# Kernel tuning notes

Hardware: AMD Instinct MI355X
Metric: run time of the kernel (lower is better)

The kernel has to match this reference:

```python
import jax, jax.numpy as jnp
import numpy as np

HIDDEN = 1024
N_HEADS = 16
HEAD = HIDDEN // N_HEADS  # 64
DFF = 4 * HIDDEN


def setup_inputs() -> dict:
    key = jax.random.key(0)
    ks = jax.random.split(key, 12)
    B, T = 4, 2048
    s = 0.02
    return {
        "x": jax.random.normal(ks[0], (B, T, HIDDEN), jnp.float32),
        # per-head QKV weights, stacked: [H, HIDDEN, HEAD] (no bias, as in Head)
        "Wq": jax.random.normal(ks[1], (N_HEADS, HIDDEN, HEAD), jnp.float32) * s,
        "Wk": jax.random.normal(ks[2], (N_HEADS, HIDDEN, HEAD), jnp.float32) * s,
        "Wv": jax.random.normal(ks[3], (N_HEADS, HIDDEN, HEAD), jnp.float32) * s,
        "Wo": jax.random.normal(ks[4], (HIDDEN, HIDDEN), jnp.float32) * s,
        "bo": jnp.zeros((HIDDEN,), jnp.float32),
        "W1": jax.random.normal(ks[5], (HIDDEN, DFF), jnp.float32) * s,
        "b1": jnp.zeros((DFF,), jnp.float32),
        "W2": jax.random.normal(ks[6], (DFF, HIDDEN), jnp.float32) * s,
        "b2": jnp.zeros((HIDDEN,), jnp.float32),
        "g1": jnp.ones((HIDDEN,), jnp.float32),
        "be1": jnp.zeros((HIDDEN,), jnp.float32),
        "g2": jnp.ones((HIDDEN,), jnp.float32),
        "be2": jnp.zeros((HIDDEN,), jnp.float32),
    }


def _layernorm(x, g, b, eps=1e-5):
    mu = jnp.mean(x, axis=-1, keepdims=True)
    var = jnp.mean(jnp.square(x - mu), axis=-1, keepdims=True)
    return (x - mu) * jax.lax.rsqrt(var + eps) * g + b


def _attention(h, Wq, Wk, Wv, Wo, bo):
    B, T, C = h.shape
    # [B,T,C] x [H,C,D] -> [B,H,T,D]
    Q = jnp.einsum('btc,hcd->bhtd', h, Wq)
    K = jnp.einsum('btc,hcd->bhtd', h, Wk)
    V = jnp.einsum('btc,hcd->bhtd', h, Wv)
    scores = jnp.einsum('bhtd,bhsd->bhts', Q, K) / np.sqrt(HEAD).astype(np.float32)
    causal = jnp.tril(jnp.ones((T, T), bool))
    scores = jnp.where(causal, scores, -jnp.inf)
    attn = jax.nn.softmax(scores, axis=-1)
    out = jnp.einsum('bhts,bhsd->bhtd', attn, V)
    # concat heads in order (head axis -> last dim blocks)
    out = out.transpose(0, 2, 1, 3).reshape(B, T, C)
    return out @ Wo + bo


def reference(x, Wq, Wk, Wv, Wo, bo, W1, b1, W2, b2, g1, be1, g2, be2):
    x = x + _attention(_layernorm(x, g1, be1), Wq, Wk, Wv, Wo, bo)
    h = _layernorm(x, g2, be2)
    ff = jax.nn.relu(h @ W1 + b1) @ W2 + b2
    return x + ff
```

## Files before the change

### kernel.cpp

```cpp
#include <hip/hip_runtime.h>
#include <hip/hip_bf16.h>
#include <stdint.h>


#define HID 1024
#define NH 16
#define HD 64
#define DFF 4096
#define BATCH 4
#define SEQ 2048
#define NTOK (BATCH*SEQ)

typedef unsigned short u16;
typedef __attribute__((ext_vector_type(4))) float f32x4;
typedef __attribute__((ext_vector_type(8))) __bf16 bf16x8;

__device__ __forceinline__ u16 f2bf(float f) {
    unsigned int u = __float_as_uint(f);
    u = (u + 0x7fffu + ((u >> 16) & 1u)) >> 16;
    return (u16)u;
}

__device__ __forceinline__ void gload_lds16(const void* g, void* lds) {
    __builtin_amdgcn_global_load_lds(
        (const __attribute__((address_space(1))) unsigned int*)(uintptr_t)g,
        (__attribute__((address_space(3))) unsigned int*)(uintptr_t)lds, 16, 0, 0);
}

__global__ __launch_bounds__(256) void ln_kernel(const float* __restrict__ x,
                                                 const float* __restrict__ g,
                                                 const float* __restrict__ be,
                                                 u16* __restrict__ out) {
    __shared__ float red[10];
    const int row = blockIdx.x, tid = threadIdx.x;
    const float4 v = ((const float4*)(x + (size_t)row * HID))[tid];
    float s  = v.x + v.y + v.z + v.w;
    float s2 = v.x*v.x + v.y*v.y + v.z*v.z + v.w*v.w;
    for (int off = 32; off > 0; off >>= 1) {
        s  += __shfl_down(s, off, 64);
        s2 += __shfl_down(s2, off, 64);
    }
    if ((tid & 63) == 0) { red[tid >> 6] = s; red[4 + (tid >> 6)] = s2; }
    __syncthreads();
    if (tid == 0) {
        red[8] = red[0] + red[1] + red[2] + red[3];
        red[9] = red[4] + red[5] + red[6] + red[7];
    }
    __syncthreads();
    const float mu  = red[8] * (1.f / HID);
    const float var = red[9] * (1.f / HID) - mu * mu;
    const float rstd = rsqrtf(var + 1e-5f);
    const float4 g4 = ((const float4*)g)[tid];
    const float4 b4 = ((const float4*)be)[tid];
    ushort4 o;
    o.x = f2bf((v.x - mu) * rstd * g4.x + b4.x);
    o.y = f2bf((v.y - mu) * rstd * g4.y + b4.y);
    o.z = f2bf((v.z - mu) * rstd * g4.z + b4.z);
    o.w = f2bf((v.w - mu) * rstd * g4.w + b4.w);
    ((ushort4*)(out + (size_t)row * HID))[tid] = o;
}

__global__ __launch_bounds__(256) void transpose_w(const float* __restrict__ in,
                                                   u16* __restrict__ out, int R, int C) {
    __shared__ float t[32][33];
    const int r0 = blockIdx.x * 32, c0 = blockIdx.y * 32;
    const float* inb = in + (size_t)blockIdx.z * R * C;
    u16* outb = out + (size_t)blockIdx.z * R * C;
    const int tid = threadIdx.x;
    const int tr = tid >> 3, tc = (tid & 7) * 4;
    const float4 v = *(const float4*)&inb[(size_t)(r0 + tr) * C + c0 + tc];
    t[tr][tc] = v.x; t[tr][tc + 1] = v.y; t[tr][tc + 2] = v.z; t[tr][tc + 3] = v.w;
    __syncthreads();
    ushort4 o;
    o.x = f2bf(t[tc + 0][tr]);
    o.y = f2bf(t[tc + 1][tr]);
    o.z = f2bf(t[tc + 2][tr]);
    o.w = f2bf(t[tc + 3][tr]);
    *(ushort4*)&outb[(size_t)(c0 + tr) * R + r0 + tc] = o;
}

__global__ __launch_bounds__(256) void transpose_v(const u16* __restrict__ in,
                                                   u16* __restrict__ out) {
    __shared__ u16 t[64][65];
    const int s0 = blockIdx.x * 64;
    const size_t bh = blockIdx.y;
    const u16* inb = in + bh * SEQ * HD;
    u16* outb = out + bh * HD * SEQ;
    const int tid = threadIdx.x;
    const int r = tid >> 2, c = (tid & 3) * 16;
    bf16x8 a = *(const bf16x8*)&inb[(size_t)(s0 + r) * HD + c];
    bf16x8 b = *(const bf16x8*)&inb[(size_t)(s0 + r) * HD + c + 8];
    #pragma unroll
    for (int i = 0; i < 8; i++) {
        t[r][c + i]     = ((const u16*)&a)[i];
        t[r][c + 8 + i] = ((const u16*)&b)[i];
    }
    __syncthreads();
    u16 o0[8], o1[8];
    #pragma unroll
    for (int i = 0; i < 8; i++) { o0[i] = t[c + i][r]; o1[i] = t[c + 8 + i][r]; }
    *(bf16x8*)&outb[(size_t)r * SEQ + s0 + c]     = *(const bf16x8*)o0;
    *(bf16x8*)&outb[(size_t)r * SEQ + s0 + c + 8] = *(const bf16x8*)o1;
}

template <int MODE>
__global__ __launch_bounds__(256) void gemm_kernel(const u16* __restrict__ A,
                                                   const u16* __restrict__ B,
                                                   float* __restrict__ outf,
                                                   u16* __restrict__ outh,
                                                   const float* __restrict__ bias,
                                                   const float* __restrict__ resid,
                                                   int K, int N, float scale) {
    __shared__ u16 Al[128][32];
    __shared__ u16 Bl[128][32];
    const int tid = threadIdx.x;
    const int w = tid >> 6, l = tid & 63;
    const int wr = w >> 1, wc = w & 1;
    const int m0 = blockIdx.x * 128, n0 = blockIdx.y * 128;

    f32x4 acc[4][4] = {};

    const u16* Ag = A + (size_t)(m0 + w * 32) * K;
    const u16* Bg = B + (size_t)(n0 + w * 32) * K;
    const int lr = l >> 2;
    const int lc = (l & 3) * 8;

    for (int k0 = 0; k0 < K; k0 += 32) {
        __syncthreads();
        #pragma unroll
        for (int it = 0; it < 2; it++) {
            gload_lds16(Ag + (size_t)(it * 16 + lr) * K + k0 + lc, &Al[w * 32 + it * 16][0]);
            gload_lds16(Bg + (size_t)(it * 16 + lr) * K + k0 + lc, &Bl[w * 32 + it * 16][0]);
        }
        __syncthreads();
        bf16x8 af[4], bf[4];
        #pragma unroll
        for (int i = 0; i < 4; i++)
            af[i] = *(const bf16x8*)&Al[wr * 64 + i * 16 + (l & 15)][(l >> 4) * 8];
        #pragma unroll
        for (int i = 0; i < 4; i++)
            bf[i] = *(const bf16x8*)&Bl[wc * 64 + i * 16 + (l & 15)][(l >> 4) * 8];
        #pragma unroll
        for (int mi = 0; mi < 4; mi++)
            #pragma unroll
            for (int nj = 0; nj < 4; nj++)
                acc[mi][nj] = __builtin_amdgcn_mfma_f32_16x16x32_bf16(af[mi], bf[nj], acc[mi][nj], 0, 0, 0);
    }

    const int r00 = m0 + wr * 64 + ((l >> 4) << 2);
    const int c00 = n0 + wc * 64 + (l & 15);
    if (MODE == 0) {
        #pragma unroll
        for (int nj = 0; nj < 4; nj++) {
            const int c = c00 + nj * 16;
            const int h = c >> 6, d = c & 63;
            #pragma unroll
            for (int mi = 0; mi < 4; mi++)
                #pragma unroll
                for (int j = 0; j < 4; j++) {
                    const int r = r00 + mi * 16 + j;
                    const int b = r >> 11, t = r & (SEQ - 1);
                    outh[((size_t)(b * NH + h) * SEQ + t) * HD + d] = f2bf(acc[mi][nj][j] * scale);
                }
        }
    } else if (MODE == 1) {
        #pragma unroll
        for (int nj = 0; nj < 4; nj++) {
            const int c = c00 + nj * 16;
            const float bi = bias[c];
            #pragma unroll
            for (int mi = 0; mi < 4; mi++)
                #pragma unroll
                for (int j = 0; j < 4; j++) {
                    const int r = r00 + mi * 16 + j;
                    const size_t idx = (size_t)r * N + c;
                    outf[idx] = resid[idx] + acc[mi][nj][j] + bi;
                }
        }
    } else {
        #pragma unroll
        for (int nj = 0; nj < 4; nj++) {
            const int c = c00 + nj * 16;
            const float bi = bias[c];
            #pragma unroll
            for (int mi = 0; mi < 4; mi++)
                #pragma unroll
                for (int j = 0; j < 4; j++) {
                    const int r = r00 + mi * 16 + j;
                    const float v = acc[mi][nj][j] + bi;
                    outh[(size_t)r * N + c] = f2bf(v > 0.f ? v : 0.f);
                }
        }
    }
}

__global__ __launch_bounds__(256) void attn_kernel(const u16* __restrict__ Q,
                                                   const u16* __restrict__ K,
                                                   const u16* __restrict__ Vt,
                                                   u16* __restrict__ O) {
    __shared__ u16 Kl[64 * 64];
    __shared__ u16 Vl[64 * 64];
    __shared__ u16 Pl[4][16 * 64];
    const int qt = blockIdx.x, bh = blockIdx.y;
    const int tid = threadIdx.x, w = tid >> 6, l = tid & 63;
    const int g = l >> 4, c16 = l & 15;

    const u16* Qg = Q + ((size_t)bh * SEQ + qt * 64 + w * 16) * HD;
    bf16x8 qf[2];
    qf[0] = *(const bf16x8*)&Qg[(size_t)c16 * HD + g * 8];
    qf[1] = *(const bf16x8*)&Qg[(size_t)c16 * HD + 32 + g * 8];

    f32x4 o[4] = {};
    float mrow[4], lrow[4];
    #pragma unroll
    for (int j = 0; j < 4; j++) { mrow[j] = -1e30f; lrow[j] = 0.f; }

    char* KlB = (char*)Kl;
    char* VlB = (char*)Vl;
    char* PlB = (char*)&Pl[w][0];

    for (int st = 0; st <= qt; ++st) {
        __syncthreads();
        {
            const u16* Kg = K + ((size_t)bh * SEQ + st * 64) * HD;
            const u16* Vg = Vt + (size_t)bh * HD * SEQ + st * 64;
            #pragma unroll
            for (int it = 0; it < 2; it++) {
                const int idx = it * 256 + tid;
                const int r = idx >> 3;
                const int cb = (idx & 7) * 16;
                bf16x8 kv = *(const bf16x8*)((const char*)Kg + (size_t)r * 128 + cb);
                *(bf16x8*)(KlB + r * 128 + (cb ^ ((r & 7) << 4))) = kv;
                bf16x8 vv = *(const bf16x8*)((const char*)Vg + (size_t)r * (SEQ * 2) + cb);
                *(bf16x8*)(VlB + r * 128 + (cb ^ ((r & 7) << 4))) = vv;
            }
        }
        __syncthreads();

        f32x4 s[4];
        #pragma unroll
        for (int n = 0; n < 4; n++) {
            const int row = n * 16 + c16;
            const char* base = KlB + row * 128;
            bf16x8 b0 = *(const bf16x8*)(base + ((g * 16) ^ ((row & 7) << 4)));
            bf16x8 b1 = *(const bf16x8*)(base + ((64 + g * 16) ^ ((row & 7) << 4)));
            f32x4 z = {};
            z = __builtin_amdgcn_mfma_f32_16x16x32_bf16(qf[0], b0, z, 0, 0, 0);
            s[n] = __builtin_amdgcn_mfma_f32_16x16x32_bf16(qf[1], b1, z, 0, 0, 0);
        }
        if (st == qt) {
            #pragma unroll
            for (int n = 0; n < 4; n++)
                #pragma unroll
                for (int j = 0; j < 4; j++) {
                    const int ql = w * 16 + g * 4 + j, sl = n * 16 + c16;
                    if (sl > ql) s[n][j] = -1e30f;
                }
        }
        #pragma unroll
        for (int j = 0; j < 4; j++) {
            float mx = fmaxf(fmaxf(s[0][j], s[1][j]), fmaxf(s[2][j], s[3][j]));
            for (int off = 1; off < 16; off <<= 1) mx = fmaxf(mx, __shfl_xor(mx, off, 64));
            const float newm = fmaxf(mrow[j], mx);
            const float sc = __expf(mrow[j] - newm);
            mrow[j] = newm;
            float ps = 0.f;
            #pragma unroll
            for (int n = 0; n < 4; n++) {
                const float p = __expf(s[n][j] - newm);
                s[n][j] = p; ps += p;
            }
            for (int off = 1; off < 16; off <<= 1) ps += __shfl_xor(ps, off, 64);
            lrow[j] = lrow[j] * sc + ps;
            #pragma unroll
            for (int n = 0; n < 4; n++) o[n][j] *= sc;
        }
        #pragma unroll
        for (int n = 0; n < 4; n++)
            #pragma unroll
            for (int j = 0; j < 4; j++) {
                const int row = g * 4 + j;
                const int cb = (n * 16 + c16) * 2;
                *(u16*)(PlB + row * 128 + (cb ^ ((row & 7) << 4))) = f2bf(s[n][j]);
            }
        bf16x8 pa[2];
        #pragma unroll
        for (int kb = 0; kb < 2; kb++) {
            const int row = c16;
            pa[kb] = *(const bf16x8*)(PlB + row * 128 + ((kb * 64 + g * 16) ^ ((row & 7) << 4)));
        }
        #pragma unroll
        for (int n = 0; n < 4; n++) {
            const int row = n * 16 + c16;
            const char* base = VlB + row * 128;
            bf16x8 v0 = *(const bf16x8*)(base + ((g * 16) ^ ((row & 7) << 4)));
            bf16x8 v1 = *(const bf16x8*)(base + ((64 + g * 16) ^ ((row & 7) << 4)));
            o[n] = __builtin_amdgcn_mfma_f32_16x16x32_bf16(pa[0], v0, o[n], 0, 0, 0);
            o[n] = __builtin_amdgcn_mfma_f32_16x16x32_bf16(pa[1], v1, o[n], 0, 0, 0);
        }
    }

    const int b = bh >> 4, h = bh & 15;
    #pragma unroll
    for (int j = 0; j < 4; j++) {
        const float inv = 1.f / lrow[j];
        const int t = qt * 64 + w * 16 + g * 4 + j;
        #pragma unroll
        for (int n = 0; n < 4; n++)
            O[((size_t)b * SEQ + t) * HID + h * HD + n * 16 + c16] = f2bf(o[n][j] * inv);
    }
}

extern "C" void kernel_launch(void* const* d_in, const int* in_sizes, int n_in,
                              void* d_out, int out_size, void* d_ws, size_t ws_size,
                              hipStream_t stream) {
    (void)in_sizes; (void)n_in; (void)out_size; (void)ws_size;
    const float* x   = (const float*)d_in[0];
    const float* Wq  = (const float*)d_in[1];
    const float* Wk  = (const float*)d_in[2];
    const float* Wv  = (const float*)d_in[3];
    const float* Wo  = (const float*)d_in[4];
    const float* bo  = (const float*)d_in[5];
    const float* W1  = (const float*)d_in[6];
    const float* b1  = (const float*)d_in[7];
    const float* W2  = (const float*)d_in[8];
    const float* b2  = (const float*)d_in[9];
    const float* g1  = (const float*)d_in[10];
    const float* be1 = (const float*)d_in[11];
    const float* g2  = (const float*)d_in[12];
    const float* be2 = (const float*)d_in[13];
    float* out = (float*)d_out;

    char* ws = (char*)d_ws;
    size_t off = 0;
    auto alloc = [&](size_t bytes) { void* p = ws + off; off += bytes; return p; };
    u16* Wq_t = (u16*)alloc((size_t)HID * HID * 2);
    u16* Wk_t = (u16*)alloc((size_t)HID * HID * 2);
    u16* Wv_t = (u16*)alloc((size_t)HID * HID * 2);
    u16* Wo_t = (u16*)alloc((size_t)HID * HID * 2);
    u16* W1_t = (u16*)alloc((size_t)DFF * HID * 2);
    u16* W2_t = (u16*)alloc((size_t)HID * DFF * 2);
    u16* h1   = (u16*)alloc((size_t)NTOK * HID * 2);
    u16* Qb   = (u16*)alloc((size_t)NTOK * HID * 2);
    u16* Kb   = (u16*)alloc((size_t)NTOK * HID * 2);
    u16* Vb   = (u16*)alloc((size_t)NTOK * HID * 2);
    u16* Vt   = (u16*)alloc((size_t)NTOK * HID * 2);
    float* x2 = (float*)alloc((size_t)NTOK * HID * 4);
    u16* ff1  = Qb;

    transpose_w<<<dim3(32, 2, 16), 256, 0, stream>>>(Wq, Wq_t, HID, HD);
    transpose_w<<<dim3(32, 2, 16), 256, 0, stream>>>(Wk, Wk_t, HID, HD);
    transpose_w<<<dim3(32, 2, 16), 256, 0, stream>>>(Wv, Wv_t, HID, HD);
    transpose_w<<<dim3(32, 32, 1), 256, 0, stream>>>(Wo, Wo_t, HID, HID);
    transpose_w<<<dim3(32, 128, 1), 256, 0, stream>>>(W1, W1_t, HID, DFF);
    transpose_w<<<dim3(128, 32, 1), 256, 0, stream>>>(W2, W2_t, DFF, HID);

    ln_kernel<<<NTOK, 256, 0, stream>>>(x, g1, be1, h1);

    gemm_kernel<0><<<dim3(64, 8), 256, 0, stream>>>(h1, Wq_t, nullptr, Qb, nullptr, nullptr, HID, HID, 0.125f);
    gemm_kernel<0><<<dim3(64, 8), 256, 0, stream>>>(h1, Wk_t, nullptr, Kb, nullptr, nullptr, HID, HID, 1.0f);
    gemm_kernel<0><<<dim3(64, 8), 256, 0, stream>>>(h1, Wv_t, nullptr, Vb, nullptr, nullptr, HID, HID, 1.0f);

    transpose_v<<<dim3(SEQ / 64, BATCH * NH), 256, 0, stream>>>(Vb, Vt);

    u16* attn_out = Vb;
    attn_kernel<<<dim3(SEQ / 64, BATCH * NH), 256, 0, stream>>>(Qb, Kb, Vt, attn_out);

    gemm_kernel<1><<<dim3(64, 8), 256, 0, stream>>>(attn_out, Wo_t, x2, nullptr, bo, x, HID, HID, 1.f);

    ln_kernel<<<NTOK, 256, 0, stream>>>(x2, g2, be2, h1);

    gemm_kernel<2><<<dim3(64, 32), 256, 0, stream>>>(h1, W1_t, nullptr, ff1, b1, nullptr, HID, DFF, 1.f);

    gemm_kernel<1><<<dim3(64, 8), 256, 0, stream>>>(ff1, W2_t, out, nullptr, b2, x2, DFF, HID, 1.f);
}
```

Before: 696.5 us.

## Add 256x256 double-buffered GEMM, fuse QKV projection, prefetch attention K/V tiles

Adds a new 512-thread GEMM kernel with 256x256 tiles, a 64-wide K step and double-buffered LDS via direct global-to-LDS loads. It also adds XCD-aware block remapping and s_setprio around the MFMA bursts. The three QKV projections are fused into one GEMM over a concatenated weight. The new kernel also replaces the W1 GEMM, aiming to raise MFMA utilisation and cut launch and reload overhead. Attention now double-buffers K/V tiles through registers so the next tile's global loads overlap compute, at the cost of more LDS and registers.

```diff
diff --git a/kernel.cpp b/kernel.cpp
--- a/kernel.cpp
+++ b/kernel.cpp
@@ -133,37 +133,23 @@
             gload_lds16(Bg + (size_t)(it * 16 + lr) * K + k0 + lc, &Bl[w * 32 + it * 16][0]);
         }
         __syncthreads();
-        bf16x8 af[4], bf[4];
+        bf16x8 af[4], bfr[4];
         #pragma unroll
         for (int i = 0; i < 4; i++)
             af[i] = *(const bf16x8*)&Al[wr * 64 + i * 16 + (l & 15)][(l >> 4) * 8];
         #pragma unroll
         for (int i = 0; i < 4; i++)
-            bf[i] = *(const bf16x8*)&Bl[wc * 64 + i * 16 + (l & 15)][(l >> 4) * 8];
+            bfr[i] = *(const bf16x8*)&Bl[wc * 64 + i * 16 + (l & 15)][(l >> 4) * 8];
         #pragma unroll
         for (int mi = 0; mi < 4; mi++)
             #pragma unroll
             for (int nj = 0; nj < 4; nj++)
-                acc[mi][nj] = __builtin_amdgcn_mfma_f32_16x16x32_bf16(af[mi], bf[nj], acc[mi][nj], 0, 0, 0);
+                acc[mi][nj] = __builtin_amdgcn_mfma_f32_16x16x32_bf16(af[mi], bfr[nj], acc[mi][nj], 0, 0, 0);
     }
 
     const int r00 = m0 + wr * 64 + ((l >> 4) << 2);
     const int c00 = n0 + wc * 64 + (l & 15);
-    if (MODE == 0) {
-        #pragma unroll
-        for (int nj = 0; nj < 4; nj++) {
-            const int c = c00 + nj * 16;
-            const int h = c >> 6, d = c & 63;
-            #pragma unroll
-            for (int mi = 0; mi < 4; mi++)
-                #pragma unroll
-                for (int j = 0; j < 4; j++) {
-                    const int r = r00 + mi * 16 + j;
-                    const int b = r >> 11, t = r & (SEQ - 1);
-                    outh[((size_t)(b * NH + h) * SEQ + t) * HD + d] = f2bf(acc[mi][nj][j] * scale);
-                }
-        }
-    } else if (MODE == 1) {
+    if (MODE == 1) {
         #pragma unroll
         for (int nj = 0; nj < 4; nj++) {
             const int c = c00 + nj * 16;
@@ -194,12 +180,145 @@
     }
 }
 
+template <int MODE>
+__global__ __launch_bounds__(512, 2) void gemm256(const u16* __restrict__ A,
+                                                  const u16* __restrict__ B,
+                                                  float* __restrict__ outf,
+                                                  u16* __restrict__ outh,
+                                                  const float* __restrict__ bias,
+                                                  const float* __restrict__ resid,
+                                                  int K, int N, int nbn) {
+    __shared__ char lds[131072];
+    const int tid = threadIdx.x;
+    const int w = tid >> 6, l = tid & 63;
+    const int wr = w >> 2, wc = w & 3;
+    const int l15 = l & 15, lg = l >> 4;
+
+    const int nwg = gridDim.x;
+    int wg;
+    {
+        const int q = nwg >> 3, r = nwg & 7;
+        const int xcd = blockIdx.x & 7, lid = blockIdx.x >> 3;
+        wg = (xcd < r ? xcd * (q + 1) : r * (q + 1) + (xcd - r) * q) + lid;
+    }
+    const int nbm = nwg / nbn;
+    const int m0 = (wg % nbm) * 256;
+    const int n0 = (wg / nbm) * 256;
+
+    const size_t Kb = (size_t)K * 2;
+    const int NT = K >> 6;
+
+    f32x4 acc[8][4] = {};
+
+    auto stage_half = [&](int q, int nxt, int k0) {
+        const char* G = (const char*)((q & 2) ? B : A);
+        const int row0 = ((q & 2) ? n0 : m0) + (q & 1) * 128;
+        char* halfBase = lds + nxt * 65536 + (q & 2) * 16384 + (q & 1) * 16384;
+        const int w64 = w << 6;
+        #pragma unroll
+        for (int it = 0; it < 2; ++it) {
+            const int d = (it * 512 + tid) * 16;
+            const int cb = (d & 127) ^ (((d >> 9) & 1) << 5);
+            const char* g = G + (size_t)(row0 + (d >> 7)) * Kb + (size_t)k0 * 2 + cb;
+            gload_lds16(g, halfBase + it * 8192 + w64 * 16);
+        }
+    };
+
+    #pragma unroll
+    for (int q = 0; q < 4; ++q) stage_half(q, 0, 0);
+    asm volatile("s_waitcnt vmcnt(0)" ::: "memory");
+    __builtin_amdgcn_s_barrier();
+
+    for (int t = 0; t < NT; ++t) {
+        const int cur = t & 1;
+        const char* lbA = lds + cur * 65536;
+        const char* lbB = lbA + 32768;
+        const bool pf = (t + 1 < NT);
+        #pragma unroll
+        for (int q = 0; q < 4; ++q) {
+            const int mh = q >> 1, nh = q & 1;
+            bf16x8 af[4][2], bfr[2][2];
+            #pragma unroll
+            for (int mi = 0; mi < 4; ++mi)
+                #pragma unroll
+                for (int ks = 0; ks < 2; ++ks) {
+                    const int row = wr * 128 + (mh * 4 + mi) * 16 + l15;
+                    const int cb = ks * 64 + lg * 16;
+                    af[mi][ks] = *(const bf16x8*)(lbA + row * 128 + (cb ^ (((row >> 2) & 1) << 5)));
+                }
+            #pragma unroll
+            for (int nj = 0; nj < 2; ++nj)
+                #pragma unroll
+                for (int ks = 0; ks < 2; ++ks) {
+                    const int row = wc * 64 + (nh * 2 + nj) * 16 + l15;
+                    const int cb = ks * 64 + lg * 16;
+                    bfr[nj][ks] = *(const bf16x8*)(lbB + row * 128 + (cb ^ (((row >> 2) & 1) << 5)));
+                }
+            if (pf) stage_half(q, cur ^ 1, (t + 1) << 6);
+            __builtin_amdgcn_s_barrier();
+            asm volatile("s_waitcnt lgkmcnt(0)" ::: "memory");
+            __builtin_amdgcn_sched_barrier(0);
+            __builtin_amdgcn_s_setprio(1);
+            #pragma unroll
+            for (int mi = 0; mi < 4; ++mi)
+                #pragma unroll
+                for (int nj = 0; nj < 2; ++nj)
+                    #pragma unroll
+                    for (int ks = 0; ks < 2; ++ks)
+                        acc[mh * 4 + mi][nh * 2 + nj] = __builtin_amdgcn_mfma_f32_16x16x32_bf16(
+                            af[mi][ks], bfr[nj][ks], acc[mh * 4 + mi][nh * 2 + nj], 0, 0, 0);
+            __builtin_amdgcn_s_setprio(0);
+            if (q == 3 && pf) asm volatile("s_waitcnt vmcnt(0)" ::: "memory");
+            __builtin_amdgcn_s_barrier();
+        }
+    }
+
+    #pragma unroll
+    for (int nj = 0; nj < 4; ++nj) {
+        const int c = n0 + wc * 64 + nj * 16 + l15;
+        if (MODE == 0) {
+            const int which = c >> 10, hc = c & 1023;
+            const int h = hc >> 6, d = hc & 63;
+            const float scale = (which == 0) ? 0.125f : 1.0f;
+            u16* outp = outh + (size_t)which * ((size_t)NTOK * HID);
+            #pragma unroll
+            for (int mi = 0; mi < 8; ++mi)
+                #pragma unroll
+                for (int j = 0; j < 4; ++j) {
+                    const int r = m0 + wr * 128 + mi * 16 + (lg << 2) + j;
+                    const int b = r >> 11, tt = r & (SEQ - 1);
+                    outp[((size_t)(b * NH + h) * SEQ + tt) * HD + d] = f2bf(acc[mi][nj][j] * scale);
+                }
+        } else if (MODE == 1) {
+            const float bi = bias[c];
+            #pragma unroll
+            for (int mi = 0; mi < 8; ++mi)
+                #pragma unroll
+                for (int j = 0; j < 4; ++j) {
+                    const int r = m0 + wr * 128 + mi * 16 + (lg << 2) + j;
+                    const size_t idx = (size_t)r * N + c;
+                    outf[idx] = resid[idx] + acc[mi][nj][j] + bi;
+                }
+        } else {
+            const float bi = bias[c];
+            #pragma unroll
+            for (int mi = 0; mi < 8; ++mi)
+                #pragma unroll
+                for (int j = 0; j < 4; ++j) {
+                    const int r = m0 + wr * 128 + mi * 16 + (lg << 2) + j;
+                    const float v = acc[mi][nj][j] + bi;
+                    outh[(size_t)r * N + c] = f2bf(v > 0.f ? v : 0.f);
+                }
+        }
+    }
+}
+
 __global__ __launch_bounds__(256) void attn_kernel(const u16* __restrict__ Q,
                                                    const u16* __restrict__ K,
                                                    const u16* __restrict__ Vt,
                                                    u16* __restrict__ O) {
-    __shared__ u16 Kl[64 * 64];
-    __shared__ u16 Vl[64 * 64];
+    __shared__ u16 Kl[2][64 * 64];
+    __shared__ u16 Vl[2][64 * 64];
     __shared__ u16 Pl[4][16 * 64];
     const int qt = blockIdx.x, bh = blockIdx.y;
     const int tid = threadIdx.x, w = tid >> 6, l = tid & 63;
@@ -215,29 +334,46 @@
     #pragma unroll
     for (int j = 0; j < 4; j++) { mrow[j] = -1e30f; lrow[j] = 0.f; }
 
-    char* KlB = (char*)Kl;
-    char* VlB = (char*)Vl;
+    const u16* Kg0 = K + (size_t)bh * SEQ * HD;
+    const u16* Vg0 = Vt + (size_t)bh * HD * SEQ;
+    const int sr = tid >> 2;
+    const int scb = (tid & 3) * 32;
     char* PlB = (char*)&Pl[w][0];
 
+    bf16x8 kreg[2], vreg[2];
+    auto load_tile = [&](int st) {
+        const char* Kg = (const char*)(Kg0 + (size_t)st * 64 * HD);
+        const char* Vg = (const char*)(Vg0 + st * 64);
+        #pragma unroll
+        for (int it = 0; it < 2; it++) {
+            kreg[it] = *(const bf16x8*)(Kg + (size_t)sr * 128 + scb + it * 16);
+            vreg[it] = *(const bf16x8*)(Vg + (size_t)sr * (SEQ * 2) + scb + it * 16);
+        }
+    };
+    auto write_tile = [&](int buf) {
+        char* KlB = (char*)Kl[buf];
+        char* VlB = (char*)Vl[buf];
+        const int sw = (sr & 7) << 4;
+        #pragma unroll
+        for (int it = 0; it < 2; it++) {
+            *(bf16x8*)(KlB + sr * 128 + ((scb + it * 16) ^ sw)) = kreg[it];
+            *(bf16x8*)(VlB + sr * 128 + ((scb + it * 16) ^ sw)) = vreg[it];
+        }
+    };
+
+    load_tile(0);
+    write_tile(0);
+
     for (int st = 0; st <= qt; ++st) {
+        const int cur = st & 1;
         __syncthreads();
-        {
-            const u16* Kg = K + ((size_t)bh * SEQ + st * 64) * HD;
-            const u16* Vg = Vt + (size_t)bh * HD * SEQ + st * 64;
-            #pragma unroll
-            for (int it = 0; it < 2; it++) {
-                const int idx = it * 256 + tid;
-                const int r = idx >> 3;
-                const int cb = (idx & 7) * 16;
-                bf16x8 kv = *(const bf16x8*)((const char*)Kg + (size_t)r * 128 + cb);
-                *(bf16x8*)(KlB + r * 128 + (cb ^ ((r & 7) << 4))) = kv;
-                bf16x8 vv = *(const bf16x8*)((const char*)Vg + (size_t)r * (SEQ * 2) + cb);
-                *(bf16x8*)(VlB + r * 128 + (cb ^ ((r & 7) << 4))) = vv;
-            }
-        }
-        __syncthreads();
+        const bool pf = (st + 1 <= qt);
+        if (pf) load_tile(st + 1);
+        const char* KlB = (const char*)Kl[cur];
+        const char* VlB = (const char*)Vl[cur];
 
         f32x4 s[4];
+        __builtin_amdgcn_s_setprio(1);
         #pragma unroll
         for (int n = 0; n < 4; n++) {
             const int row = n * 16 + c16;
@@ -248,6 +384,7 @@
             z = __builtin_amdgcn_mfma_f32_16x16x32_bf16(qf[0], b0, z, 0, 0, 0);
             s[n] = __builtin_amdgcn_mfma_f32_16x16x32_bf16(qf[1], b1, z, 0, 0, 0);
         }
+        __builtin_amdgcn_s_setprio(0);
         if (st == qt) {
             #pragma unroll
             for (int n = 0; n < 4; n++)
@@ -285,10 +422,9 @@
             }
         bf16x8 pa[2];
         #pragma unroll
-        for (int kb = 0; kb < 2; kb++) {
-            const int row = c16;
-            pa[kb] = *(const bf16x8*)(PlB + row * 128 + ((kb * 64 + g * 16) ^ ((row & 7) << 4)));
-        }
+        for (int kb = 0; kb < 2; kb++)
+            pa[kb] = *(const bf16x8*)(PlB + c16 * 128 + ((kb * 64 + g * 16) ^ ((c16 & 7) << 4)));
+        __builtin_amdgcn_s_setprio(1);
         #pragma unroll
         for (int n = 0; n < 4; n++) {
             const int row = n * 16 + c16;
@@ -298,6 +434,8 @@
             o[n] = __builtin_amdgcn_mfma_f32_16x16x32_bf16(pa[0], v0, o[n], 0, 0, 0);
             o[n] = __builtin_amdgcn_mfma_f32_16x16x32_bf16(pa[1], v1, o[n], 0, 0, 0);
         }
+        __builtin_amdgcn_s_setprio(0);
+        if (pf) write_tile(cur ^ 1);
     }
 
     const int b = bh >> 4, h = bh & 15;
@@ -334,9 +472,7 @@
     char* ws = (char*)d_ws;
     size_t off = 0;
     auto alloc = [&](size_t bytes) { void* p = ws + off; off += bytes; return p; };
-    u16* Wq_t = (u16*)alloc((size_t)HID * HID * 2);
-    u16* Wk_t = (u16*)alloc((size_t)HID * HID * 2);
-    u16* Wv_t = (u16*)alloc((size_t)HID * HID * 2);
+    u16* Wqkv_t = (u16*)alloc((size_t)3 * HID * HID * 2);
     u16* Wo_t = (u16*)alloc((size_t)HID * HID * 2);
     u16* W1_t = (u16*)alloc((size_t)DFF * HID * 2);
     u16* W2_t = (u16*)alloc((size_t)HID * DFF * 2);
@@ -347,19 +483,19 @@
     u16* Vt   = (u16*)alloc((size_t)NTOK * HID * 2);
     float* x2 = (float*)alloc((size_t)NTOK * HID * 4);
     u16* ff1  = Qb;
-
-    transpose_w<<<dim3(32, 2, 16), 256, 0, stream>>>(Wq, Wq_t, HID, HD);
-    transpose_w<<<dim3(32, 2, 16), 256, 0, stream>>>(Wk, Wk_t, HID, HD);
-    transpose_w<<<dim3(32, 2, 16), 256, 0, stream>>>(Wv, Wv_t, HID, HD);
+    (void)Kb; (void)Vt;
+
+    transpose_w<<<dim3(32, 2, 16), 256, 0, stream>>>(Wq, Wqkv_t, HID, HD);
+    transpose_w<<<dim3(32, 2, 16), 256, 0, stream>>>(Wk, Wqkv_t + (size_t)HID * HID, HID, HD);
+    transpose_w<<<dim3(32, 2, 16), 256, 0, stream>>>(Wv, Wqkv_t + (size_t)2 * HID * HID, HID, HD);
     transpose_w<<<dim3(32, 32, 1), 256, 0, stream>>>(Wo, Wo_t, HID, HID);
     transpose_w<<<dim3(32, 128, 1), 256, 0, stream>>>(W1, W1_t, HID, DFF);
     transpose_w<<<dim3(128, 32, 1), 256, 0, stream>>>(W2, W2_t, DFF, HID);
 
     ln_kernel<<<NTOK, 256, 0, stream>>>(x, g1, be1, h1);
 
-    gemm_kernel<0><<<dim3(64, 8), 256, 0, stream>>>(h1, Wq_t, nullptr, Qb, nullptr, nullptr, HID, HID, 0.125f);
-    gemm_kernel<0><<<dim3(64, 8), 256, 0, stream>>>(h1, Wk_t, nullptr, Kb, nullptr, nullptr, HID, HID, 1.0f);
-    gemm_kernel<0><<<dim3(64, 8), 256, 0, stream>>>(h1, Wv_t, nullptr, Vb, nullptr, nullptr, HID, HID, 1.0f);
+    gemm256<0><<<dim3((NTOK / 256) * (3072 / 256)), 512, 0, stream>>>(
+        h1, Wqkv_t, nullptr, Qb, nullptr, nullptr, HID, 3072, 3072 / 256);
 
     transpose_v<<<dim3(SEQ / 64, BATCH * NH), 256, 0, stream>>>(Vb, Vt);
 
@@ -370,7 +506,8 @@
 
     ln_kernel<<<NTOK, 256, 0, stream>>>(x2, g2, be2, h1);
 
-    gemm_kernel<2><<<dim3(64, 32), 256, 0, stream>>>(h1, W1_t, nullptr, ff1, b1, nullptr, HID, DFF, 1.f);
+    gemm256<2><<<dim3((NTOK / 256) * (DFF / 256)), 512, 0, stream>>>(
+        h1, W1_t, nullptr, ff1, b1, nullptr, HID, DFF, DFF / 256);
 
     gemm_kernel<1><<<dim3(64, 8), 256, 0, stream>>>(ff1, W2_t, out, nullptr, b2, x2, DFF, HID, 1.f);
 }
```

Measured after the change: 723.8 us. +3.9%, slower.
